# Optimization experiments

Hardware: AMD Instinct MI355X
Metric: run time of the kernel (lower is better)

## Reference

```python
import jax, jax.numpy as jnp
import numpy as np

N = 50000   # nodes
E = 800000  # edges (avg degree 16)
IN, H, OUT = 128, 256, 40


def setup_inputs() -> dict:
    key = jax.random.key(0)
    ks = jax.random.split(key, 7)
    x = jax.random.normal(ks[0], (N, IN), dtype=jnp.float32)
    edge_index = jax.random.randint(ks[1], (2, E), 0, N, dtype=jnp.int32)
    def w(k, fi, fo):
        return jax.random.normal(k, (fi, fo), dtype=jnp.float32) / np.sqrt(fi).astype(np.float32)
    return {
        "x": x,
        "edge_index": edge_index,
        "W0": w(ks[2], IN, H), "b0": jnp.zeros((H,), jnp.float32),
        "W1": w(ks[3], H, H),  "b1": jnp.zeros((H,), jnp.float32),
        "W2": w(ks[4], H, H),  "b2": jnp.zeros((H,), jnp.float32),
        "Wh": w(ks[5], H, OUT), "bh": jnp.zeros((OUT,), jnp.float32),
    }


def gcn_conv(x, src, dst, W, b, n):
    """PyG GCNConv: self-loops + symmetric D^-1/2 (A+I) D^-1/2 normalization."""
    h = x @ W  # [N, Fout]
    # degree with self-loop (edge weights are all 1)
    deg = jnp.ones((n,), h.dtype).at[dst].add(1.0)
    inv = jax.lax.rsqrt(deg)  # deg^{-1/2}
    coef = inv[src] * inv[dst]  # [E]
    agg = jax.ops.segment_sum(h[src] * coef[:, None], dst, num_segments=n)
    agg = agg + h * (inv * inv)[:, None]  # self-loop contribution
    return agg + b


def reference(x, edge_index, W0, b0, W1, b1, W2, b2, Wh, bh):
    src, dst = edge_index[0], edge_index[1]
    h = jax.nn.relu(gcn_conv(x, src, dst, W0, b0, N))   # conv0 + relu (dropout p=0)
    h = jax.nn.relu(gcn_conv(h, src, dst, W1, b1, N))   # conv1 + relu
    h = gcn_conv(h, src, dst, W2, b2, N)                # final conv (no relu)
    g = jnp.mean(h, axis=0, keepdims=True)              # batch=None -> global mean, [1, H]
    return g @ Wh + bh                                  # prediction head, [1, OUT]
```

## Files before the change

### kernel.cpp

```cpp
#include <hip/hip_runtime.h>

#define NN 50000
#define NE 800000
#define FIN 128
#define FH 256
#define FOUT 40
#define NPAD 50432
#define NN2 50048
#define NB 256
#define BSPAN 196
#define EBLK 4096
#define NBLK_A 196
#define NVP 64

typedef float f32x4 __attribute__((ext_vector_type(4)));
typedef short bf16x8 __attribute__((ext_vector_type(8)));

__device__ __forceinline__ ushort f2bf(float f) {
    unsigned u = __float_as_uint(f);
    unsigned r = (u + 0x7FFFu + ((u >> 16) & 1u)) >> 16;
    return (ushort)r;
}
__device__ __forceinline__ float bf2f(ushort b) {
    return __uint_as_float(((unsigned)b) << 16);
}


__global__ __launch_bounds__(256) void bucket_cnt_kernel(const int* __restrict__ dst,
                                                         int* __restrict__ bcnt) {
    __shared__ int h[NB];
    const int t = threadIdx.x;
    h[t] = 0;
    __syncthreads();
    const int e0 = blockIdx.x * EBLK;
    const int n  = min(EBLK, NE - e0);
    for (int i = t; i < n; i += 256)
        atomicAdd(&h[dst[e0 + i] / BSPAN], 1);
    __syncthreads();
    if (h[t] > 0) atomicAdd(&bcnt[t], h[t]);
}

__global__ __launch_bounds__(256) void bucket_scan_kernel(const int* __restrict__ bcnt,
                                                          int* __restrict__ bbase,
                                                          int* __restrict__ bcur) {
    __shared__ int sh[256];
    int t = threadIdx.x;
    int v = bcnt[t];
    sh[t] = v;
    __syncthreads();
    #pragma unroll
    for (int off = 1; off < 256; off <<= 1) {
        int u = (t >= off) ? sh[t - off] : 0;
        __syncthreads();
        sh[t] += u;
        __syncthreads();
    }
    int excl = sh[t] - v;
    bbase[t] = excl;
    bcur[t]  = excl;
    if (t == 255) bbase[256] = sh[255];
}

__global__ __launch_bounds__(256) void binA_kernel(const int* __restrict__ src,
                                                   const int* __restrict__ dst,
                                                   int* __restrict__ bcur,
                                                   unsigned* __restrict__ inter) {
    __shared__ int hcnt[NB];
    __shared__ int hoff[NB];
    __shared__ int lcur[NB];
    __shared__ int gbase[NB];
    __shared__ unsigned stage[EBLK];

    const int t  = threadIdx.x;
    const int e0 = blockIdx.x * EBLK;
    const int n  = min(EBLK, NE - e0);

    hcnt[t] = 0;
    __syncthreads();
    for (int i = t; i < n; i += 256)
        atomicAdd(&hcnt[dst[e0 + i] / BSPAN], 1);
    __syncthreads();
    int v = hcnt[t];
    hoff[t] = v;
    __syncthreads();
    #pragma unroll
    for (int off = 1; off < NB; off <<= 1) {
        int u = (t >= off) ? hoff[t - off] : 0;
        __syncthreads();
        hoff[t] += u;
        __syncthreads();
    }
    int excl = hoff[t] - v;
    __syncthreads();
    hoff[t] = excl;
    lcur[t] = excl;
    if (v > 0) gbase[t] = atomicAdd(&bcur[t], v);
    __syncthreads();
    for (int i = t; i < n; i += 256) {
        int d = dst[e0 + i];
        int s = src[e0 + i];
        int b = d / BSPAN;
        int idx = atomicAdd(&lcur[b], 1);
        stage[idx] = ((unsigned)d << 16) | (unsigned)s;
    }
    __syncthreads();
    for (int i = t; i < n; i += 256) {
        unsigned rec = stage[i];
        int b = (int)(rec >> 16) / BSPAN;
        inter[gbase[b] + (i - hoff[b])] = rec;
    }
}

__global__ __launch_bounds__(256) void binB1_kernel(const unsigned* __restrict__ inter,
                                                    const int* __restrict__ bbase,
                                                    int* __restrict__ row_start,
                                                    float* __restrict__ inv,
                                                    float* __restrict__ wsum) {
    __shared__ int lcnt[BSPAN];
    __shared__ int sh[256];
    const int b   = blockIdx.x;
    const int nlo = b * BSPAN;
    const int nhi = min(nlo + BSPAN, NN);
    const int nn  = nhi - nlo;
    const int base = bbase[b];
    const int cnt  = bbase[b + 1] - base;
    const int t = threadIdx.x;

    for (int i = t; i < nn; i += 256) lcnt[i] = 0;
    __syncthreads();
    for (int i = t; i < cnt; i += 256)
        atomicAdd(&lcnt[(int)(inter[base + i] >> 16) - nlo], 1);
    __syncthreads();
    int c = (t < nn) ? lcnt[t] : 0;
    sh[t] = c;
    __syncthreads();
    #pragma unroll
    for (int off = 1; off < 256; off <<= 1) {
        int u = (t >= off) ? sh[t - off] : 0;
        __syncthreads();
        sh[t] += u;
        __syncthreads();
    }
    if (t < nn) {
        row_start[nlo + t] = base + sh[t] - c;
        inv[nlo + t]  = rsqrtf((float)(c + 1));
        wsum[nlo + t] = 0.0f;
    }
    if (b == NB - 1 && t == 0) row_start[NN] = NE;
}

__global__ __launch_bounds__(256) void binB2_kernel(const unsigned* __restrict__ inter,
                                                    const int* __restrict__ bbase,
                                                    const int* __restrict__ row_start,
                                                    const float* __restrict__ inv,
                                                    float2* __restrict__ edata,
                                                    float* __restrict__ wsum) {
    __shared__ int lcur[BSPAN];
    const int b   = blockIdx.x;
    const int nlo = b * BSPAN;
    const int nhi = min(nlo + BSPAN, NN);
    const int nn  = nhi - nlo;
    const int base = bbase[b];
    const int cnt  = bbase[b + 1] - base;
    const int t = threadIdx.x;

    for (int i = t; i < nn; i += 256) lcur[i] = row_start[nlo + i];
    __syncthreads();
    for (int i = t; i < cnt; i += 256) {
        unsigned rec = inter[base + i];
        int d = (int)(rec >> 16);
        int s = (int)(rec & 0xFFFFu);
        float coef = inv[s] * inv[d];
        int pos = atomicAdd(&lcur[d - nlo], 1);
        edata[pos] = make_float2(__int_as_float(s), coef);
        unsafeAtomicAdd(&wsum[s], coef);
    }
}


__global__ void prep_kernel(const float* __restrict__ W0, const float* __restrict__ W1,
                            const float* __restrict__ x,
                            ushort* __restrict__ W0tH, ushort* __restrict__ W0tL,
                            ushort* __restrict__ W1tH, ushort* __restrict__ xb) {
    int t = blockIdx.x * 256 + threadIdx.x;
    if (t < NN2 * 32) {
        int row = t >> 5;
        int c4  = t & 31;
        ushort4 o = make_ushort4(0, 0, 0, 0);
        if (row < NN) {
            float4 v = *reinterpret_cast<const float4*>(x + (size_t)row * FIN + c4 * 4);
            o = make_ushort4(f2bf(v.x), f2bf(v.y), f2bf(v.z), f2bf(v.w));
        }
        *reinterpret_cast<ushort4*>(xb + (size_t)row * FIN + c4 * 4) = o;
    }
    if (t < FIN * FH) {
        int n = t % FH;
        int k = t / FH;
        float f = W0[t];
        ushort h = f2bf(f);
        W0tH[n * FIN + k] = h;
        W0tL[n * FIN + k] = f2bf(f - bf2f(h));
    } else if (t < FIN * FH + FH * FH) {
        int j = t - FIN * FH;
        int n = j % FH;
        int k = j / FH;
        W1tH[n * FH + k] = f2bf(W1[j]);
    }
}


template<int TERMS, bool BIAS_RELU>
__global__ __launch_bounds__(256) void gemm_mfma_kernel(
    const ushort* __restrict__ AH, const ushort* __restrict__ AL,
    const ushort* __restrict__ BH, const ushort* __restrict__ BL,
    const float* __restrict__ bias,
    ushort* __restrict__ outB,
    int K) {
    constexpr int NARR = (TERMS == 3) ? 2 : 1;
    __shared__ ushort smem[(128 + 256) * 40 * NARR];
    ushort* Ah = smem;
    ushort* Bh = smem + 128 * 40;
    ushort* Al = (TERMS == 3) ? smem + 384 * 40 : nullptr;
    ushort* Bl = (TERMS == 3) ? smem + 384 * 40 + 128 * 40 : nullptr;

    const int tid  = threadIdx.x;
    const int lane = tid & 63;
    const int w    = tid >> 6;
    const int wr   = w >> 1;
    const int wc   = w & 1;
    const int row0 = blockIdx.x * 128;

    f32x4 acc[4][8] = {};

    for (int k0 = 0; k0 < K; k0 += 32) {
        #pragma unroll
        for (int i = 0; i < 2; ++i) {
            int c  = i * 256 + tid;
            int r  = c >> 2;
            int cb = c & 3;
            *reinterpret_cast<uint4*>(&Ah[r * 40 + cb * 8]) =
                *reinterpret_cast<const uint4*>(AH + (size_t)(row0 + r) * K + k0 + cb * 8);
            if (TERMS == 3)
                *reinterpret_cast<uint4*>(&Al[r * 40 + cb * 8]) =
                    *reinterpret_cast<const uint4*>(AL + (size_t)(row0 + r) * K + k0 + cb * 8);
        }
        #pragma unroll
        for (int i = 0; i < 4; ++i) {
            int c  = i * 256 + tid;
            int r  = c >> 2;
            int cb = c & 3;
            *reinterpret_cast<uint4*>(&Bh[r * 40 + cb * 8]) =
                *reinterpret_cast<const uint4*>(BH + (size_t)r * K + k0 + cb * 8);
            if (TERMS == 3)
                *reinterpret_cast<uint4*>(&Bl[r * 40 + cb * 8]) =
                    *reinterpret_cast<const uint4*>(BL + (size_t)r * K + k0 + cb * 8);
        }
        __syncthreads();

        const int rsel = lane & 15;
        const int ksel = (lane >> 4) * 8;
        bf16x8 ah[4], bh[8];
        #pragma unroll
        for (int m = 0; m < 4; ++m)
            ah[m] = *reinterpret_cast<const bf16x8*>(&Ah[(wr * 64 + m * 16 + rsel) * 40 + ksel]);
        #pragma unroll
        for (int n = 0; n < 8; ++n)
            bh[n] = *reinterpret_cast<const bf16x8*>(&Bh[(wc * 128 + n * 16 + rsel) * 40 + ksel]);

        if (TERMS == 3) {
            bf16x8 al[4], bl[8];
            #pragma unroll
            for (int m = 0; m < 4; ++m)
                al[m] = *reinterpret_cast<const bf16x8*>(&Al[(wr * 64 + m * 16 + rsel) * 40 + ksel]);
            #pragma unroll
            for (int n = 0; n < 8; ++n)
                bl[n] = *reinterpret_cast<const bf16x8*>(&Bl[(wc * 128 + n * 16 + rsel) * 40 + ksel]);
            #pragma unroll
            for (int m = 0; m < 4; ++m)
                #pragma unroll
                for (int n = 0; n < 8; ++n) {
                    acc[m][n] = __builtin_amdgcn_mfma_f32_16x16x32_bf16(ah[m], bh[n], acc[m][n], 0, 0, 0);
                    acc[m][n] = __builtin_amdgcn_mfma_f32_16x16x32_bf16(ah[m], bl[n], acc[m][n], 0, 0, 0);
                    acc[m][n] = __builtin_amdgcn_mfma_f32_16x16x32_bf16(al[m], bh[n], acc[m][n], 0, 0, 0);
                }
        } else {
            #pragma unroll
            for (int m = 0; m < 4; ++m)
                #pragma unroll
                for (int n = 0; n < 8; ++n)
                    acc[m][n] = __builtin_amdgcn_mfma_f32_16x16x32_bf16(ah[m], bh[n], acc[m][n], 0, 0, 0);
        }
        __syncthreads();
    }

    const int cl = lane & 15;
    const int rg = lane >> 4;
    float bn[8];
    if (BIAS_RELU) {
        #pragma unroll
        for (int n = 0; n < 8; ++n) bn[n] = bias[wc * 128 + n * 16 + cl];
    }
    #pragma unroll
    for (int m = 0; m < 4; ++m) {
        #pragma unroll
        for (int i = 0; i < 4; ++i) {
            int gr = row0 + wr * 64 + m * 16 + rg * 4 + i;
            #pragma unroll
            for (int n = 0; n < 8; ++n) {
                int gc = wc * 128 + n * 16 + cl;
                float o = acc[m][n][i];
                if (BIAS_RELU) o = fmaxf(o + bn[n], 0.0f);
                outB[(size_t)gr * FH + gc] = f2bf(o);
            }
        }
    }
}


__global__ __launch_bounds__(256) void gather_x_kernel(const ushort* __restrict__ xb,
                                                       const float2* __restrict__ edata,
                                                       const int* __restrict__ row_start,
                                                       const float* __restrict__ inv,
                                                       ushort* __restrict__ outH,
                                                       ushort* __restrict__ outL) {
    int node = blockIdx.x * 4 + (threadIdx.x >> 6);
    int lane = threadIdx.x & 63;
    if (node >= NN2) return;
    size_t o = (size_t)node * FIN + lane * 2;
    if (node >= NN) {
        *reinterpret_cast<ushort2*>(outH + o) = make_ushort2(0, 0);
        *reinterpret_cast<ushort2*>(outL + o) = make_ushort2(0, 0);
        return;
    }

    int beg = row_start[node];
    int end = row_start[node + 1];

    float iv = inv[node];
    float c  = iv * iv;
    ushort2 sv = *reinterpret_cast<const ushort2*>(xb + o);
    float2 a0 = make_float2(bf2f(sv.x) * c, bf2f(sv.y) * c);
    float2 a1 = make_float2(0.f, 0.f);
    float2 a2 = make_float2(0.f, 0.f);
    float2 a3 = make_float2(0.f, 0.f);

    int i = beg;
    if ((i & 1) && i < end) {
        float2 ed = edata[i];
        ushort2 u = *reinterpret_cast<const ushort2*>(xb + (size_t)__float_as_int(ed.x) * FIN + lane * 2);
        a0.x += bf2f(u.x) * ed.y; a0.y += bf2f(u.y) * ed.y;
        ++i;
    }
    for (; i + 8 <= end; i += 8) {
        float4 e01 = *reinterpret_cast<const float4*>(&edata[i]);
        float4 e23 = *reinterpret_cast<const float4*>(&edata[i + 2]);
        float4 e45 = *reinterpret_cast<const float4*>(&edata[i + 4]);
        float4 e67 = *reinterpret_cast<const float4*>(&edata[i + 6]);
        ushort2 u0 = *reinterpret_cast<const ushort2*>(xb + (size_t)__float_as_int(e01.x) * FIN + lane * 2);
        ushort2 u1 = *reinterpret_cast<const ushort2*>(xb + (size_t)__float_as_int(e01.z) * FIN + lane * 2);
        ushort2 u2 = *reinterpret_cast<const ushort2*>(xb + (size_t)__float_as_int(e23.x) * FIN + lane * 2);
        ushort2 u3 = *reinterpret_cast<const ushort2*>(xb + (size_t)__float_as_int(e23.z) * FIN + lane * 2);
        ushort2 u4 = *reinterpret_cast<const ushort2*>(xb + (size_t)__float_as_int(e45.x) * FIN + lane * 2);
        ushort2 u5 = *reinterpret_cast<const ushort2*>(xb + (size_t)__float_as_int(e45.z) * FIN + lane * 2);
        ushort2 u6 = *reinterpret_cast<const ushort2*>(xb + (size_t)__float_as_int(e67.x) * FIN + lane * 2);
        ushort2 u7 = *reinterpret_cast<const ushort2*>(xb + (size_t)__float_as_int(e67.z) * FIN + lane * 2);
        a0.x += bf2f(u0.x) * e01.y; a0.y += bf2f(u0.y) * e01.y;
        a1.x += bf2f(u1.x) * e01.w; a1.y += bf2f(u1.y) * e01.w;
        a2.x += bf2f(u2.x) * e23.y; a2.y += bf2f(u2.y) * e23.y;
        a3.x += bf2f(u3.x) * e23.w; a3.y += bf2f(u3.y) * e23.w;
        a0.x += bf2f(u4.x) * e45.y; a0.y += bf2f(u4.y) * e45.y;
        a1.x += bf2f(u5.x) * e45.w; a1.y += bf2f(u5.y) * e45.w;
        a2.x += bf2f(u6.x) * e67.y; a2.y += bf2f(u6.y) * e67.y;
        a3.x += bf2f(u7.x) * e67.w; a3.y += bf2f(u7.y) * e67.w;
    }
    for (; i + 2 <= end; i += 2) {
        float4 e01 = *reinterpret_cast<const float4*>(&edata[i]);
        ushort2 u0 = *reinterpret_cast<const ushort2*>(xb + (size_t)__float_as_int(e01.x) * FIN + lane * 2);
        ushort2 u1 = *reinterpret_cast<const ushort2*>(xb + (size_t)__float_as_int(e01.z) * FIN + lane * 2);
        a0.x += bf2f(u0.x) * e01.y; a0.y += bf2f(u0.y) * e01.y;
        a1.x += bf2f(u1.x) * e01.w; a1.y += bf2f(u1.y) * e01.w;
    }
    if (i < end) {
        float2 ed = edata[i];
        ushort2 u = *reinterpret_cast<const ushort2*>(xb + (size_t)__float_as_int(ed.x) * FIN + lane * 2);
        a0.x += bf2f(u.x) * ed.y; a0.y += bf2f(u.y) * ed.y;
    }

    float ax = a0.x + a1.x + a2.x + a3.x;
    float ay = a0.y + a1.y + a2.y + a3.y;
    ushort h0 = f2bf(ax), h1 = f2bf(ay);
    ushort l0 = f2bf(ax - bf2f(h0)), l1 = f2bf(ay - bf2f(h1));
    *reinterpret_cast<ushort2*>(outH + o) = make_ushort2(h0, h1);
    *reinterpret_cast<ushort2*>(outL + o) = make_ushort2(l0, l1);
}


__global__ __launch_bounds__(256) void gather_colsum_kernel(const ushort* __restrict__ lin,
                                                            const float2* __restrict__ edata,
                                                            const int* __restrict__ row_start,
                                                            const float* __restrict__ inv,
                                                            const float* __restrict__ wsum,
                                                            const float* __restrict__ bias,
                                                            float* __restrict__ vpart) {
    __shared__ float sh[4][256];
    const int wid  = threadIdx.x >> 6;
    const int lane = threadIdx.x & 63;
    const int node = blockIdx.x * 4 + wid;

    int beg = row_start[node];
    int end = row_start[node + 1];

    float iv = inv[node];
    float c  = iv * iv;
    ushort4 sv = *reinterpret_cast<const ushort4*>(lin + (size_t)node * FH + lane * 4);
    float4 b = *reinterpret_cast<const float4*>(bias + lane * 4);
    float4 a0 = make_float4(bf2f(sv.x) * c + b.x, bf2f(sv.y) * c + b.y,
                            bf2f(sv.z) * c + b.z, bf2f(sv.w) * c + b.w);
    float4 a1 = make_float4(0.f, 0.f, 0.f, 0.f);
    float4 a2 = make_float4(0.f, 0.f, 0.f, 0.f);
    float4 a3 = make_float4(0.f, 0.f, 0.f, 0.f);

    int i = beg;
    if ((i & 1) && i < end) {
        float2 ed = edata[i];
        float cf = ed.y;
        ushort4 wv = *reinterpret_cast<const ushort4*>(lin + (size_t)__float_as_int(ed.x) * FH + lane * 4);
        a0.x += bf2f(wv.x) * cf; a0.y += bf2f(wv.y) * cf;
        a0.z += bf2f(wv.z) * cf; a0.w += bf2f(wv.w) * cf;
        ++i;
    }
    for (; i + 8 <= end; i += 8) {
        float4 e01 = *reinterpret_cast<const float4*>(&edata[i]);
        float4 e23 = *reinterpret_cast<const float4*>(&edata[i + 2]);
        float4 e45 = *reinterpret_cast<const float4*>(&edata[i + 4]);
        float4 e67 = *reinterpret_cast<const float4*>(&edata[i + 6]);
        ushort4 w0 = *reinterpret_cast<const ushort4*>(lin + (size_t)__float_as_int(e01.x) * FH + lane * 4);
        ushort4 w1 = *reinterpret_cast<const ushort4*>(lin + (size_t)__float_as_int(e01.z) * FH + lane * 4);
        ushort4 w2 = *reinterpret_cast<const ushort4*>(lin + (size_t)__float_as_int(e23.x) * FH + lane * 4);
        ushort4 w3 = *reinterpret_cast<const ushort4*>(lin + (size_t)__float_as_int(e23.z) * FH + lane * 4);
        ushort4 w4 = *reinterpret_cast<const ushort4*>(lin + (size_t)__float_as_int(e45.x) * FH + lane * 4);
        ushort4 w5 = *reinterpret_cast<const ushort4*>(lin + (size_t)__float_as_int(e45.z) * FH + lane * 4);
        ushort4 w6 = *reinterpret_cast<const ushort4*>(lin + (size_t)__float_as_int(e67.x) * FH + lane * 4);
        ushort4 w7 = *reinterpret_cast<const ushort4*>(lin + (size_t)__float_as_int(e67.z) * FH + lane * 4);
        a0.x += bf2f(w0.x) * e01.y; a0.y += bf2f(w0.y) * e01.y;
        a0.z += bf2f(w0.z) * e01.y; a0.w += bf2f(w0.w) * e01.y;
        a1.x += bf2f(w1.x) * e01.w; a1.y += bf2f(w1.y) * e01.w;
        a1.z += bf2f(w1.z) * e01.w; a1.w += bf2f(w1.w) * e01.w;
        a2.x += bf2f(w2.x) * e23.y; a2.y += bf2f(w2.y) * e23.y;
        a2.z += bf2f(w2.z) * e23.y; a2.w += bf2f(w2.w) * e23.y;
        a3.x += bf2f(w3.x) * e23.w; a3.y += bf2f(w3.y) * e23.w;
        a3.z += bf2f(w3.z) * e23.w; a3.w += bf2f(w3.w) * e23.w;
        a0.x += bf2f(w4.x) * e45.y; a0.y += bf2f(w4.y) * e45.y;
        a0.z += bf2f(w4.z) * e45.y; a0.w += bf2f(w4.w) * e45.y;
        a1.x += bf2f(w5.x) * e45.w; a1.y += bf2f(w5.y) * e45.w;
        a1.z += bf2f(w5.z) * e45.w; a1.w += bf2f(w5.w) * e45.w;
        a2.x += bf2f(w6.x) * e67.y; a2.y += bf2f(w6.y) * e67.y;
        a2.z += bf2f(w6.z) * e67.y; a2.w += bf2f(w6.w) * e67.y;
        a3.x += bf2f(w7.x) * e67.w; a3.y += bf2f(w7.y) * e67.w;
        a3.z += bf2f(w7.z) * e67.w; a3.w += bf2f(w7.w) * e67.w;
    }
    for (; i + 2 <= end; i += 2) {
        float4 e01 = *reinterpret_cast<const float4*>(&edata[i]);
        ushort4 w0 = *reinterpret_cast<const ushort4*>(lin + (size_t)__float_as_int(e01.x) * FH + lane * 4);
        ushort4 w1 = *reinterpret_cast<const ushort4*>(lin + (size_t)__float_as_int(e01.z) * FH + lane * 4);
        a0.x += bf2f(w0.x) * e01.y; a0.y += bf2f(w0.y) * e01.y;
        a0.z += bf2f(w0.z) * e01.y; a0.w += bf2f(w0.w) * e01.y;
        a1.x += bf2f(w1.x) * e01.w; a1.y += bf2f(w1.y) * e01.w;
        a1.z += bf2f(w1.z) * e01.w; a1.w += bf2f(w1.w) * e01.w;
    }
    if (i < end) {
        float2 ed = edata[i];
        float cf = ed.y;
        ushort4 wv = *reinterpret_cast<const ushort4*>(lin + (size_t)__float_as_int(ed.x) * FH + lane * 4);
        a0.x += bf2f(wv.x) * cf; a0.y += bf2f(wv.y) * cf;
        a0.z += bf2f(wv.z) * cf; a0.w += bf2f(wv.w) * cf;
    }

    float wn = wsum[node] + c;
    float4 vp = make_float4(fmaxf(a0.x + a1.x + a2.x + a3.x, 0.f) * wn,
                            fmaxf(a0.y + a1.y + a2.y + a3.y, 0.f) * wn,
                            fmaxf(a0.z + a1.z + a2.z + a3.z, 0.f) * wn,
                            fmaxf(a0.w + a1.w + a2.w + a3.w, 0.f) * wn);

    *reinterpret_cast<float4*>(&sh[wid][lane * 4]) = vp;
    __syncthreads();
    if (wid == 0) {
        float4 s1 = *reinterpret_cast<const float4*>(&sh[1][lane * 4]);
        float4 s2 = *reinterpret_cast<const float4*>(&sh[2][lane * 4]);
        float4 s3 = *reinterpret_cast<const float4*>(&sh[3][lane * 4]);
        float* vp_out = vpart + (size_t)(blockIdx.x & (NVP - 1)) * FH;
        unsafeAtomicAdd(&vp_out[lane * 4 + 0], vp.x + s1.x + s2.x + s3.x);
        unsafeAtomicAdd(&vp_out[lane * 4 + 1], vp.y + s1.y + s2.y + s3.y);
        unsafeAtomicAdd(&vp_out[lane * 4 + 2], vp.z + s1.z + s2.z + s3.z);
        unsafeAtomicAdd(&vp_out[lane * 4 + 3], vp.w + s1.w + s2.w + s3.w);
    }
}

__global__ __launch_bounds__(256) void head2_kernel(const float* __restrict__ vpart,
                                                    const float* __restrict__ W2,
                                                    const float* __restrict__ b2,
                                                    const float* __restrict__ Wh,
                                                    const float* __restrict__ bh,
                                                    float* __restrict__ out) {
    __shared__ float vsh[FH];
    __shared__ float m[FH];
    int t = threadIdx.x;
    float vf = 0.0f;
    for (int s = 0; s < NVP; ++s)
        vf += vpart[s * FH + t];
    vsh[t] = vf;
    __syncthreads();
    const float scale = 1.0f / (float)NN;
    float s = 0.0f;
    for (int f = 0; f < FH; ++f)
        s += vsh[f] * W2[f * FH + t];
    m[t] = s * scale + b2[t];
    __syncthreads();
    if (t < FOUT) {
        float o = 0.0f;
        for (int f = 0; f < FH; ++f)
            o += m[f] * Wh[f * FOUT + t];
        out[t] = o + bh[t];
    }
}


extern "C" void kernel_launch(void* const* d_in, const int* in_sizes, int n_in,
                              void* d_out, int out_size, void* d_ws, size_t ws_size,
                              hipStream_t stream) {
    const float* x   = (const float*)d_in[0];
    const int*   ei  = (const int*)d_in[1];
    const float* W0  = (const float*)d_in[2];
    const float* b0  = (const float*)d_in[3];
    const float* W1  = (const float*)d_in[4];
    const float* b1  = (const float*)d_in[5];
    const float* W2  = (const float*)d_in[6];
    const float* b2  = (const float*)d_in[7];
    const float* Wh  = (const float*)d_in[8];
    const float* bh  = (const float*)d_in[9];
    float* out = (float*)d_out;

    const int* src = ei;
    const int* dst = ei + NE;

    float*    inv       = (float*)d_ws;
    int*      row_start = (int*)(inv + NPAD);
    float*    wsum      = (float*)(row_start + NPAD);
    int*      bcnt      = (int*)(wsum + NPAD);
    float*    vpart     = (float*)(bcnt + 256);
    int*      bbase     = (int*)(vpart + NVP * FH);
    int*      bcur      = bbase + 320;
    unsigned* inter     = (unsigned*)(bcur + 256);
    float2*   edata     = (float2*)(inter + NE);
    ushort*   W0tH      = (ushort*)(edata + NE);
    ushort*   W0tL      = W0tH + 256 * 128;
    ushort*   W1tH      = W0tL + 256 * 128;
    ushort*   xb        = W1tH + 256 * 256;
    ushort*   aggxH     = xb + (size_t)NN2 * 128;
    ushort*   aggxL     = aggxH + (size_t)NN2 * 128;
    ushort*   linb      = aggxH;
    ushort*   h0H       = aggxL + (size_t)NN2 * 128;

    const int gemm_grid = NN2 / 128;
    const int nblk_gx = NN2 / 4;
    const int nblk_g  = NN / 4;

    hipMemsetAsync(bcnt, 0, (256 + NVP * FH) * sizeof(int), stream);
    bucket_cnt_kernel<<<NBLK_A, 256, 0, stream>>>(dst, bcnt);
    bucket_scan_kernel<<<1, 256, 0, stream>>>(bcnt, bbase, bcur);
    binA_kernel<<<NBLK_A, 256, 0, stream>>>(src, dst, bcur, inter);
    binB1_kernel<<<NB, 256, 0, stream>>>(inter, bbase, row_start, inv, wsum);
    binB2_kernel<<<NB, 256, 0, stream>>>(inter, bbase, row_start, inv, edata, wsum);
    prep_kernel<<<(NN2 * 32 + 255) / 256, 256, 0, stream>>>(W0, W1, x, W0tH, W0tL, W1tH, xb);

    gather_x_kernel<<<nblk_gx, 256, 0, stream>>>(xb, edata, row_start, inv, aggxH, aggxL);
    gemm_mfma_kernel<3, true><<<gemm_grid, 256, 0, stream>>>(aggxH, aggxL, W0tH, W0tL, b0,
                                                             h0H, FIN);

    gemm_mfma_kernel<1, false><<<gemm_grid, 256, 0, stream>>>(h0H, nullptr, W1tH, nullptr, nullptr,
                                                              linb, FH);

    gather_colsum_kernel<<<nblk_g, 256, 0, stream>>>(linb, edata, row_start, inv, wsum, b1, vpart);

    head2_kernel<<<1, 256, 0, stream>>>(vpart, W2, b2, Wh, bh, out);
}
```

Before: 282.8 us.

## Split gather kernels across feature slices with one element per lane

Both gather kernels now split the feature dimension across blocks: gather_x uses 2 blocks per group of 4 nodes with one bf16 per lane, and gather_colsum uses 4 blocks per 4 nodes with one feature per lane. This multiplies the block count and the thread-level parallelism for the latency-bound irregular gathers. In exchange, each edge's index and coefficient are loaded 2-4 times, per-lane loads shrink to 2-byte scalars, and colsum issues more atomics.

```diff
diff --git a/kernel.cpp b/kernel.cpp
--- a/kernel.cpp
+++ b/kernel.cpp
@@ -323,13 +323,15 @@
                                                        const float* __restrict__ inv,
                                                        ushort* __restrict__ outH,
                                                        ushort* __restrict__ outL) {
-    int node = blockIdx.x * 4 + (threadIdx.x >> 6);
-    int lane = threadIdx.x & 63;
-    if (node >= NN2) return;
-    size_t o = (size_t)node * FIN + lane * 2;
+    const int wid  = threadIdx.x >> 6;
+    const int lane = threadIdx.x & 63;
+    const int hf   = blockIdx.x & 1;
+    const int node = (blockIdx.x >> 1) * 4 + wid;
+    const int f    = hf * 64 + lane;
+    size_t o = (size_t)node * FIN + f;
     if (node >= NN) {
-        *reinterpret_cast<ushort2*>(outH + o) = make_ushort2(0, 0);
-        *reinterpret_cast<ushort2*>(outL + o) = make_ushort2(0, 0);
+        outH[o] = 0;
+        outL[o] = 0;
         return;
     }
 
@@ -338,17 +340,13 @@
 
     float iv = inv[node];
     float c  = iv * iv;
-    ushort2 sv = *reinterpret_cast<const ushort2*>(xb + o);
-    float2 a0 = make_float2(bf2f(sv.x) * c, bf2f(sv.y) * c);
-    float2 a1 = make_float2(0.f, 0.f);
-    float2 a2 = make_float2(0.f, 0.f);
-    float2 a3 = make_float2(0.f, 0.f);
+    float a0 = bf2f(xb[o]) * c;
+    float a1 = 0.f, a2 = 0.f, a3 = 0.f;
 
     int i = beg;
     if ((i & 1) && i < end) {
         float2 ed = edata[i];
-        ushort2 u = *reinterpret_cast<const ushort2*>(xb + (size_t)__float_as_int(ed.x) * FIN + lane * 2);
-        a0.x += bf2f(u.x) * ed.y; a0.y += bf2f(u.y) * ed.y;
+        a0 += bf2f(xb[(size_t)__float_as_int(ed.x) * FIN + f]) * ed.y;
         ++i;
     }
     for (; i + 8 <= end; i += 8) {
@@ -356,42 +354,38 @@
         float4 e23 = *reinterpret_cast<const float4*>(&edata[i + 2]);
         float4 e45 = *reinterpret_cast<const float4*>(&edata[i + 4]);
         float4 e67 = *reinterpret_cast<const float4*>(&edata[i + 6]);
-        ushort2 u0 = *reinterpret_cast<const ushort2*>(xb + (size_t)__float_as_int(e01.x) * FIN + lane * 2);
-        ushort2 u1 = *reinterpret_cast<const ushort2*>(xb + (size_t)__float_as_int(e01.z) * FIN + lane * 2);
-        ushort2 u2 = *reinterpret_cast<const ushort2*>(xb + (size_t)__float_as_int(e23.x) * FIN + lane * 2);
-        ushort2 u3 = *reinterpret_cast<const ushort2*>(xb + (size_t)__float_as_int(e23.z) * FIN + lane * 2);
-        ushort2 u4 = *reinterpret_cast<const ushort2*>(xb + (size_t)__float_as_int(e45.x) * FIN + lane * 2);
-        ushort2 u5 = *reinterpret_cast<const ushort2*>(xb + (size_t)__float_as_int(e45.z) * FIN + lane * 2);
-        ushort2 u6 = *reinterpret_cast<const ushort2*>(xb + (size_t)__float_as_int(e67.x) * FIN + lane * 2);
-        ushort2 u7 = *reinterpret_cast<const ushort2*>(xb + (size_t)__float_as_int(e67.z) * FIN + lane * 2);
-        a0.x += bf2f(u0.x) * e01.y; a0.y += bf2f(u0.y) * e01.y;
-        a1.x += bf2f(u1.x) * e01.w; a1.y += bf2f(u1.y) * e01.w;
-        a2.x += bf2f(u2.x) * e23.y; a2.y += bf2f(u2.y) * e23.y;
-        a3.x += bf2f(u3.x) * e23.w; a3.y += bf2f(u3.y) * e23.w;
-        a0.x += bf2f(u4.x) * e45.y; a0.y += bf2f(u4.y) * e45.y;
-        a1.x += bf2f(u5.x) * e45.w; a1.y += bf2f(u5.y) * e45.w;
-        a2.x += bf2f(u6.x) * e67.y; a2.y += bf2f(u6.y) * e67.y;
-        a3.x += bf2f(u7.x) * e67.w; a3.y += bf2f(u7.y) * e67.w;
+        ushort u0 = xb[(size_t)__float_as_int(e01.x) * FIN + f];
+        ushort u1 = xb[(size_t)__float_as_int(e01.z) * FIN + f];
+        ushort u2 = xb[(size_t)__float_as_int(e23.x) * FIN + f];
+        ushort u3 = xb[(size_t)__float_as_int(e23.z) * FIN + f];
+        ushort u4 = xb[(size_t)__float_as_int(e45.x) * FIN + f];
+        ushort u5 = xb[(size_t)__float_as_int(e45.z) * FIN + f];
+        ushort u6 = xb[(size_t)__float_as_int(e67.x) * FIN + f];
+        ushort u7 = xb[(size_t)__float_as_int(e67.z) * FIN + f];
+        a0 += bf2f(u0) * e01.y;
+        a1 += bf2f(u1) * e01.w;
+        a2 += bf2f(u2) * e23.y;
+        a3 += bf2f(u3) * e23.w;
+        a0 += bf2f(u4) * e45.y;
+        a1 += bf2f(u5) * e45.w;
+        a2 += bf2f(u6) * e67.y;
+        a3 += bf2f(u7) * e67.w;
     }
     for (; i + 2 <= end; i += 2) {
         float4 e01 = *reinterpret_cast<const float4*>(&edata[i]);
-        ushort2 u0 = *reinterpret_cast<const ushort2*>(xb + (size_t)__float_as_int(e01.x) * FIN + lane * 2);
-        ushort2 u1 = *reinterpret_cast<const ushort2*>(xb + (size_t)__float_as_int(e01.z) * FIN + lane * 2);
-        a0.x += bf2f(u0.x) * e01.y; a0.y += bf2f(u0.y) * e01.y;
-        a1.x += bf2f(u1.x) * e01.w; a1.y += bf2f(u1.y) * e01.w;
+        a0 += bf2f(xb[(size_t)__float_as_int(e01.x) * FIN + f]) * e01.y;
+        a1 += bf2f(xb[(size_t)__float_as_int(e01.z) * FIN + f]) * e01.w;
     }
     if (i < end) {
         float2 ed = edata[i];
-        ushort2 u = *reinterpret_cast<const ushort2*>(xb + (size_t)__float_as_int(ed.x) * FIN + lane * 2);
-        a0.x += bf2f(u.x) * ed.y; a0.y += bf2f(u.y) * ed.y;
-    }
-
-    float ax = a0.x + a1.x + a2.x + a3.x;
-    float ay = a0.y + a1.y + a2.y + a3.y;
-    ushort h0 = f2bf(ax), h1 = f2bf(ay);
-    ushort l0 = f2bf(ax - bf2f(h0)), l1 = f2bf(ay - bf2f(h1));
-    *reinterpret_cast<ushort2*>(outH + o) = make_ushort2(h0, h1);
-    *reinterpret_cast<ushort2*>(outL + o) = make_ushort2(l0, l1);
+        a0 += bf2f(xb[(size_t)__float_as_int(ed.x) * FIN + f]) * ed.y;
+    }
+
+    float ax = a0 + a1 + a2 + a3;
+    ushort hh = f2bf(ax);
+    ushort ll = f2bf(ax - bf2f(hh));
+    outH[o] = hh;
+    outL[o] = ll;
 }
 
 
@@ -402,31 +396,25 @@
                                                             const float* __restrict__ wsum,
                                                             const float* __restrict__ bias,
                                                             float* __restrict__ vpart) {
-    __shared__ float sh[4][256];
+    __shared__ float sh[4][64];
     const int wid  = threadIdx.x >> 6;
     const int lane = threadIdx.x & 63;
-    const int node = blockIdx.x * 4 + wid;
+    const int q    = blockIdx.x & 3;
+    const int node = (blockIdx.x >> 2) * 4 + wid;
+    const int f    = q * 64 + lane;
 
     int beg = row_start[node];
     int end = row_start[node + 1];
 
     float iv = inv[node];
     float c  = iv * iv;
-    ushort4 sv = *reinterpret_cast<const ushort4*>(lin + (size_t)node * FH + lane * 4);
-    float4 b = *reinterpret_cast<const float4*>(bias + lane * 4);
-    float4 a0 = make_float4(bf2f(sv.x) * c + b.x, bf2f(sv.y) * c + b.y,
-                            bf2f(sv.z) * c + b.z, bf2f(sv.w) * c + b.w);
-    float4 a1 = make_float4(0.f, 0.f, 0.f, 0.f);
-    float4 a2 = make_float4(0.f, 0.f, 0.f, 0.f);
-    float4 a3 = make_float4(0.f, 0.f, 0.f, 0.f);
+    float a0 = bf2f(lin[(size_t)node * FH + f]) * c + bias[f];
+    float a1 = 0.f, a2 = 0.f, a3 = 0.f;
 
     int i = beg;
     if ((i & 1) && i < end) {
         float2 ed = edata[i];
-        float cf = ed.y;
-        ushort4 wv = *reinterpret_cast<const ushort4*>(lin + (size_t)__float_as_int(ed.x) * FH + lane * 4);
-        a0.x += bf2f(wv.x) * cf; a0.y += bf2f(wv.y) * cf;
-        a0.z += bf2f(wv.z) * cf; a0.w += bf2f(wv.w) * cf;
+        a0 += bf2f(lin[(size_t)__float_as_int(ed.x) * FH + f]) * ed.y;
         ++i;
     }
     for (; i + 8 <= end; i += 8) {
@@ -434,65 +422,41 @@
         float4 e23 = *reinterpret_cast<const float4*>(&edata[i + 2]);
         float4 e45 = *reinterpret_cast<const float4*>(&edata[i + 4]);
         float4 e67 = *reinterpret_cast<const float4*>(&edata[i + 6]);
-        ushort4 w0 = *reinterpret_cast<const ushort4*>(lin + (size_t)__float_as_int(e01.x) * FH + lane * 4);
-        ushort4 w1 = *reinterpret_cast<const ushort4*>(lin + (size_t)__float_as_int(e01.z) * FH + lane * 4);
-        ushort4 w2 = *reinterpret_cast<const ushort4*>(lin + (size_t)__float_as_int(e23.x) * FH + lane * 4);
-        ushort4 w3 = *reinterpret_cast<const ushort4*>(lin + (size_t)__float_as_int(e23.z) * FH + lane * 4);
-        ushort4 w4 = *reinterpret_cast<const ushort4*>(lin + (size_t)__float_as_int(e45.x) * FH + lane * 4);
-        ushort4 w5 = *reinterpret_cast<const ushort4*>(lin + (size_t)__float_as_int(e45.z) * FH + lane * 4);
-        ushort4 w6 = *reinterpret_cast<const ushort4*>(lin + (size_t)__float_as_int(e67.x) * FH + lane * 4);
-        ushort4 w7 = *reinterpret_cast<const ushort4*>(lin + (size_t)__float_as_int(e67.z) * FH + lane * 4);
-        a0.x += bf2f(w0.x) * e01.y; a0.y += bf2f(w0.y) * e01.y;
-        a0.z += bf2f(w0.z) * e01.y; a0.w += bf2f(w0.w) * e01.y;
-        a1.x += bf2f(w1.x) * e01.w; a1.y += bf2f(w1.y) * e01.w;
-        a1.z += bf2f(w1.z) * e01.w; a1.w += bf2f(w1.w) * e01.w;
-        a2.x += bf2f(w2.x) * e23.y; a2.y += bf2f(w2.y) * e23.y;
-        a2.z += bf2f(w2.z) * e23.y; a2.w += bf2f(w2.w) * e23.y;
-        a3.x += bf2f(w3.x) * e23.w; a3.y += bf2f(w3.y) * e23.w;
-        a3.z += bf2f(w3.z) * e23.w; a3.w += bf2f(w3.w) * e23.w;
-        a0.x += bf2f(w4.x) * e45.y; a0.y += bf2f(w4.y) * e45.y;
-        a0.z += bf2f(w4.z) * e45.y; a0.w += bf2f(w4.w) * e45.y;
-        a1.x += bf2f(w5.x) * e45.w; a1.y += bf2f(w5.y) * e45.w;
-        a1.z += bf2f(w5.z) * e45.w; a1.w += bf2f(w5.w) * e45.w;
-        a2.x += bf2f(w6.x) * e67.y; a2.y += bf2f(w6.y) * e67.y;
-        a2.z += bf2f(w6.z) * e67.y; a2.w += bf2f(w6.w) * e67.y;
-        a3.x += bf2f(w7.x) * e67.w; a3.y += bf2f(w7.y) * e67.w;
-        a3.z += bf2f(w7.z) * e67.w; a3.w += bf2f(w7.w) * e67.w;
+        ushort u0 = lin[(size_t)__float_as_int(e01.x) * FH + f];
+        ushort u1 = lin[(size_t)__float_as_int(e01.z) * FH + f];
+        ushort u2 = lin[(size_t)__float_as_int(e23.x) * FH + f];
+        ushort u3 = lin[(size_t)__float_as_int(e23.z) * FH + f];
+        ushort u4 = lin[(size_t)__float_as_int(e45.x) * FH + f];
+        ushort u5 = lin[(size_t)__float_as_int(e45.z) * FH + f];
+        ushort u6 = lin[(size_t)__float_as_int(e67.x) * FH + f];
+        ushort u7 = lin[(size_t)__float_as_int(e67.z) * FH + f];
+        a0 += bf2f(u0) * e01.y;
+        a1 += bf2f(u1) * e01.w;
+        a2 += bf2f(u2) * e23.y;
+        a3 += bf2f(u3) * e23.w;
+        a0 += bf2f(u4) * e45.y;
+        a1 += bf2f(u5) * e45.w;
+        a2 += bf2f(u6) * e67.y;
+        a3 += bf2f(u7) * e67.w;
     }
     for (; i + 2 <= end; i += 2) {
         float4 e01 = *reinterpret_cast<const float4*>(&edata[i]);
-        ushort4 w0 = *reinterpret_cast<const ushort4*>(lin + (size_t)__float_as_int(e01.x) * FH + lane * 4);
-        ushort4 w1 = *reinterpret_cast<const ushort4*>(lin + (size_t)__float_as_int(e01.z) * FH + lane * 4);
-        a0.x += bf2f(w0.x) * e01.y; a0.y += bf2f(w0.y) * e01.y;
-        a0.z += bf2f(w0.z) * e01.y; a0.w += bf2f(w0.w) * e01.y;
-        a1.x += bf2f(w1.x) * e01.w; a1.y += bf2f(w1.y) * e01.w;
-        a1.z += bf2f(w1.z) * e01.w; a1.w += bf2f(w1.w) * e01.w;
+        a0 += bf2f(lin[(size_t)__float_as_int(e01.x) * FH + f]) * e01.y;
+        a1 += bf2f(lin[(size_t)__float_as_int(e01.z) * FH + f]) * e01.w;
     }
     if (i < end) {
         float2 ed = edata[i];
-        float cf = ed.y;
-        ushort4 wv = *reinterpret_cast<const ushort4*>(lin + (size_t)__float_as_int(ed.x) * FH + lane * 4);
-        a0.x += bf2f(wv.x) * cf; a0.y += bf2f(wv.y) * cf;
-        a0.z += bf2f(wv.z) * cf; a0.w += bf2f(wv.w) * cf;
+        a0 += bf2f(lin[(size_t)__float_as_int(ed.x) * FH + f]) * ed.y;
     }
 
     float wn = wsum[node] + c;
-    float4 vp = make_float4(fmaxf(a0.x + a1.x + a2.x + a3.x, 0.f) * wn,
-                            fmaxf(a0.y + a1.y + a2.y + a3.y, 0.f) * wn,
-                            fmaxf(a0.z + a1.z + a2.z + a3.z, 0.f) * wn,
-                            fmaxf(a0.w + a1.w + a2.w + a3.w, 0.f) * wn);
-
-    *reinterpret_cast<float4*>(&sh[wid][lane * 4]) = vp;
+    float vp = fmaxf(a0 + a1 + a2 + a3, 0.f) * wn;
+
+    sh[wid][lane] = vp;
     __syncthreads();
     if (wid == 0) {
-        float4 s1 = *reinterpret_cast<const float4*>(&sh[1][lane * 4]);
-        float4 s2 = *reinterpret_cast<const float4*>(&sh[2][lane * 4]);
-        float4 s3 = *reinterpret_cast<const float4*>(&sh[3][lane * 4]);
-        float* vp_out = vpart + (size_t)(blockIdx.x & (NVP - 1)) * FH;
-        unsafeAtomicAdd(&vp_out[lane * 4 + 0], vp.x + s1.x + s2.x + s3.x);
-        unsafeAtomicAdd(&vp_out[lane * 4 + 1], vp.y + s1.y + s2.y + s3.y);
-        unsafeAtomicAdd(&vp_out[lane * 4 + 2], vp.z + s1.z + s2.z + s3.z);
-        unsafeAtomicAdd(&vp_out[lane * 4 + 3], vp.w + s1.w + s2.w + s3.w);
+        float s = sh[0][lane] + sh[1][lane] + sh[2][lane] + sh[3][lane];
+        unsafeAtomicAdd(&vpart[(size_t)((blockIdx.x >> 2) & (NVP - 1)) * FH + f], s);
     }
 }
 
@@ -562,8 +526,8 @@
     ushort*   h0H       = aggxL + (size_t)NN2 * 128;
 
     const int gemm_grid = NN2 / 128;
-    const int nblk_gx = NN2 / 4;
-    const int nblk_g  = NN / 4;
+    const int nblk_gx = (NN2 / 4) * 2;
+    const int nblk_g  = NN;
 
     hipMemsetAsync(bcnt, 0, (256 + NVP * FH) * sizeof(int), stream);
     bucket_cnt_kernel<<<NBLK_A, 256, 0, stream>>>(dst, bcnt);
```

Result: slower. 340.8 us (+20.5%).
